# Kernel tuning notes

Measured on AMD Instinct MI355X. Metric: run time of the kernel, lower is better.

Reference implementation:

```python
import jax, jax.numpy as jnp
import numpy as np

B, PS, E, A, EMB, D, V, LC, TCAP = 128, 14, 2048, 512, 512, 512, 10000, 128, 26
T = TCAP - 1  # max decode length


def setup_inputs() -> dict:
    key = jax.random.key(0)
    ks = jax.random.split(key, 16)
    g = lambda k, shape: jax.random.normal(k, shape, jnp.float32) * 0.02
    cap_len = jax.random.randint(ks[2], (B, 1), 2, TCAP + 1).at[0, 0].set(TCAP)
    return {
        "encoder_out": jax.random.normal(ks[0], (B, PS, PS, E), jnp.float32),
        "encoded_captions": jax.random.randint(ks[1], (B, TCAP), 0, V),
        "caption_lengths": cap_len,
        "length_class": jax.random.randint(ks[3], (B,), 0, 3),
        "W_enc_att": g(ks[4], (E, A)), "b_enc_att": jnp.zeros((A,), jnp.float32),
        "W_dec_att": g(ks[5], (D, A)), "b_dec_att": jnp.zeros((A,), jnp.float32),
        "w_full_att": g(ks[6], (A,)), "b_full_att": jnp.zeros((), jnp.float32),
        "W_init_h": g(ks[7], (E, D)), "b_init_h": jnp.zeros((D,), jnp.float32),
        "W_init_c": g(ks[8], (E, D)), "b_init_c": jnp.zeros((D,), jnp.float32),
        "W_fbeta": g(ks[9], (D, E)), "b_fbeta": jnp.zeros((E,), jnp.float32),
        "emb_table": jax.random.uniform(ks[10], (V, EMB), jnp.float32, -0.1, 0.1),
        "lc_table": jax.random.uniform(ks[11], (3, LC), jnp.float32, -0.1, 0.1),
        "W_fc": jax.random.uniform(ks[12], (D, V), jnp.float32, -0.1, 0.1),
        "b_fc": jnp.zeros((V,), jnp.float32),
        "W_ih": g(ks[13], (EMB + E + LC, 4 * D)), "b_ih": jnp.zeros((4 * D,), jnp.float32),
        "W_hh": g(ks[14], (D, 4 * D)), "b_hh": jnp.zeros((4 * D,), jnp.float32),
    }


def reference(encoder_out, encoded_captions, caption_lengths, length_class,
              W_enc_att, b_enc_att, W_dec_att, b_dec_att, w_full_att, b_full_att,
              W_init_h, b_init_h, W_init_c, b_init_c, W_fbeta, b_fbeta,
              emb_table, lc_table, W_fc, b_fc, W_ih, b_ih, W_hh, b_hh):
    enc = encoder_out.reshape(B, -1, E)                      # [B, P, E]
    cap_len = caption_lengths[:, 0]
    sort_ind = jnp.argsort(-cap_len)                          # descending by length
    enc = enc[sort_ind]
    caps = encoded_captions[sort_ind]
    style = lc_table[length_class[sort_ind]]                  # [B, LC]
    dec_len = cap_len[sort_ind] - 1                           # [B]

    embs = emb_table[caps]                                    # [B, TCAP, EMB]
    mean_enc = enc.mean(axis=1)
    h0 = mean_enc @ W_init_h + b_init_h
    c0 = mean_enc @ W_init_c + b_init_c
    # encoder side of attention is time-invariant: precompute once
    att1 = jnp.einsum('bpe,ea->bpa', enc, W_enc_att) + b_enc_att

    def step(carry, xs):
        h, c = carry
        t, emb_t = xs
        att2 = h @ W_dec_att + b_dec_att
        e = jnp.einsum('bpa,a->bp', jax.nn.relu(att1 + att2[:, None, :]), w_full_att) + b_full_att
        alpha = jax.nn.softmax(e, axis=1)                     # [B, P]
        awe = jnp.einsum('bpe,bp->be', enc, alpha)
        gate = jax.nn.sigmoid(h @ W_fbeta + b_fbeta)
        x = jnp.concatenate([emb_t, style, gate * awe], axis=1)
        gates = x @ W_ih + b_ih + h @ W_hh + b_hh             # [B, 4D], order i,f,g,o
        i, f, g, o = jnp.split(gates, 4, axis=1)
        c_new = jax.nn.sigmoid(f) * c + jax.nn.sigmoid(i) * jnp.tanh(g)
        h_new = jax.nn.sigmoid(o) * jnp.tanh(c_new)
        preds = h_new @ W_fc + b_fc                           # dropout is identity in eval
        m = (t < dec_len)[:, None]                            # active sequences at step t
        return ((jnp.where(m, h_new, h), jnp.where(m, c_new, c)),
                (jnp.where(m, preds, 0.0), jnp.where(m, alpha, 0.0)))

    ts = jnp.arange(T)
    emb_seq = jnp.swapaxes(embs[:, :T, :], 0, 1)              # [T, B, EMB]
    _, (preds, alphas) = jax.lax.scan(step, (h0, c0), (ts, emb_seq))
    predictions = jnp.swapaxes(preds, 0, 1)                   # [B, T, V]
    alphas = jnp.swapaxes(alphas, 0, 1)                       # [B, T, P]
    return predictions, caps, dec_len, alphas, sort_ind
```

## Files before the change

### kernel.cpp

```cpp
#include <hip/hip_runtime.h>
#include <math.h>

constexpr int kB   = 128;
constexpr int kP   = 196;
constexpr int kPT  = 200;
constexpr int kE   = 2048;
constexpr int kA   = 512;
constexpr int kEMB = 512;
constexpr int kD   = 512;
constexpr int kV   = 10000;
constexpr int kLC  = 128;
constexpr int kTCAP= 26;
constexpr int kT   = 25;
constexpr int kX   = kEMB + kLC + kE;
constexpr int kXH  = kX + kD;
constexpr int kN3  = kV + kA + kE;
constexpr int kBIG = 1 << 30;
constexpr int KZ   = 5;

typedef __attribute__((ext_vector_type(8))) short bf8;
typedef __attribute__((ext_vector_type(4))) float f4;

__device__ inline float b2f(ushort u) { return __uint_as_float(((unsigned)u) << 16); }
__device__ inline ushort f2b(float f) {
    unsigned u = __float_as_uint(f);
    return (ushort)((u + 0x7fffu + ((u >> 16) & 1u)) >> 16);
}

#define SWZ(r, k) ((((r) * 32) + (k)) ^ (((r) & 7) << 3))

__global__ __launch_bounds__(128) void sort_setup(
    const int* __restrict__ caplen, const int* __restrict__ caps_in,
    const int* __restrict__ lclass, const float* __restrict__ lc_table,
    int* __restrict__ sort_ind, int* __restrict__ declen, int* __restrict__ caps_i,
    float* __restrict__ style,
    float* __restrict__ out_caps, float* __restrict__ out_declen,
    float* __restrict__ out_sortind)
{
    __shared__ int lens[kB];
    __shared__ int sind[kB];
    int i = threadIdx.x;
    lens[i] = caplen[i];
    __syncthreads();
    int li = lens[i];
    int r = 0;
    for (int j = 0; j < kB; j++) {
        int lj = lens[j];
        if (lj > li || (lj == li && j < i)) r++;
    }
    sind[r] = i;
    sort_ind[r] = i;
    out_sortind[r] = (float)i;
    __syncthreads();
    int orig = sind[i];
    int dl = lens[orig] - 1;
    declen[i] = dl;
    out_declen[i] = (float)dl;
    for (int t = 0; t < kTCAP; t++) {
        int cv = caps_in[orig * kTCAP + t];
        caps_i[i * kTCAP + t] = cv;
        out_caps[i * kTCAP + t] = (float)cv;
    }
    int lcl = lclass[orig];
    for (int k = 0; k < kLC; k++) style[i * kLC + k] = lc_table[lcl * kLC + k];
}

__global__ __launch_bounds__(256) void tcvt_kernel(
    const float* __restrict__ src, int ldsrc, int K, int N,
    ushort* __restrict__ dst, long long ldd)
{
    __shared__ float tile[32][33];
    int k0 = blockIdx.y * 32, n0 = blockIdx.x * 32;
    int tx = threadIdx.x & 31, ty = threadIdx.x >> 5;
    #pragma unroll
    for (int j = 0; j < 4; j++) {
        int k = k0 + ty + j * 8, n = n0 + tx;
        tile[ty + j * 8][tx] = (k < K && n < N) ? src[(long long)k * ldsrc + n] : 0.f;
    }
    __syncthreads();
    #pragma unroll
    for (int j = 0; j < 4; j++) {
        int n = n0 + ty + j * 8, k = k0 + tx;
        if (n < N && k < K) dst[(long long)n * ldd + k] = f2b(tile[tx][ty + j * 8]);
    }
}

__global__ __launch_bounds__(256) void bias_setup_kernel(
    const float* __restrict__ b_fc, const float* __restrict__ b_dec,
    const float* __restrict__ b_fb, const float* __restrict__ b_ih0,
    const float* __restrict__ b_ic0, const float* __restrict__ b_ih,
    const float* __restrict__ b_hh,
    float* __restrict__ bias3, float* __restrict__ bias_hc, float* __restrict__ gbias)
{
    int idx = blockIdx.x * 256 + threadIdx.x;
    if (idx < kN3) {
        float v;
        if (idx < kV) v = b_fc[idx];
        else if (idx < kV + kA) v = b_dec[idx - kV];
        else v = b_fb[idx - kV - kA];
        bias3[idx] = v;
    } else if (idx < kN3 + 1024) {
        int i = idx - kN3;
        bias_hc[i] = (i < 512) ? b_ih0[i] : b_ic0[i - 512];
    } else if (idx < kN3 + 1024 + 2048) {
        int i = idx - kN3 - 1024;
        gbias[i] = b_ih[i] + b_hh[i];
    }
}

__global__ __launch_bounds__(256) void enc_cvt_kernel(
    const float* __restrict__ enc, const int* __restrict__ sort_ind,
    ushort* __restrict__ enc_bf)
{
    long long idx4 = (long long)blockIdx.x * 256 + threadIdx.x;
    if (idx4 >= (long long)kB * kP * kE / 4) return;
    int r = (int)(idx4 >> 9);
    int cc = ((int)idx4 & 511) * 4;
    int b = r / kP, p = r - b * kP;
    long long srow = (long long)sort_ind[b] * kP + p;
    float4 v = *(const float4*)(enc + srow * kE + cc);
    ushort4 o; o.x = f2b(v.x); o.y = f2b(v.y); o.z = f2b(v.z); o.w = f2b(v.w);
    *(ushort4*)(enc_bf + (long long)r * kE + cc) = o;
}

__global__ __launch_bounds__(256) void encT_kernel(
    const ushort* __restrict__ enc_bf, ushort* __restrict__ enc_T)
{
    __shared__ ushort tile[kPT][65];
    int b = blockIdx.y, e0 = blockIdx.x * 64;
    int tid = threadIdx.x;
    tile[196 + (tid >> 6)][tid & 63] = 0;
    const ushort* src = enc_bf + (long long)b * kP * kE + e0;
    for (int idx = tid; idx < kP * 64; idx += 256) {
        int p = idx >> 6, j = idx & 63;
        tile[p][j] = src[(long long)p * kE + j];
    }
    __syncthreads();
    ushort* dst = enc_T + ((long long)b * kE + e0) * kPT;
    for (int j = 0; j < 64; j++) {
        if (tid < kPT) dst[(long long)j * kPT + tid] = tile[tid][j];
    }
}

__global__ __launch_bounds__(256) void mean_enc_kernel(
    const float* __restrict__ encf, const ushort* __restrict__ encb,
    const ushort* __restrict__ encT, int mode,
    const int* __restrict__ sort_ind, float* __restrict__ me)
{
    int idx = blockIdx.x * 256 + threadIdx.x;
    int b = idx >> 11, e = idx & 2047;
    float s = 0.f;
    if (mode == 2) {
        const ushort* base = encT + (long long)idx * kPT;
        #pragma unroll
        for (int i = 0; i < kPT / 8; i++) {
            uint4 u = *(const uint4*)(base + i * 8);
            const ushort* pu = (const ushort*)&u;
            #pragma unroll
            for (int j = 0; j < 8; j++) s += b2f(pu[j]);
        }
    } else if (mode == 1) {
        const ushort* base = encb + (long long)b * kP * kE + e;
        #pragma unroll 4
        for (int p = 0; p < kP; p++) s += b2f(base[(long long)p * kE]);
    } else {
        const float* base = encf + (long long)sort_ind[b] * kP * kE + e;
        #pragma unroll 4
        for (int p = 0; p < kP; p++) s += base[(long long)p * kE];
    }
    me[idx] = s * (1.0f / 196.0f);
}

__global__ __launch_bounds__(256) void gemm2(
    const void* __restrict__ Am, int lda, int a_bf16,
    const ushort* __restrict__ Bt, int ldbt,
    const float* __restrict__ bias,
    void* __restrict__ out1, long long ldc1, int c1_bf16,
    int split1, float* __restrict__ out2, long long ldc2,
    int split2, float* __restrict__ out3, long long ldc3,
    const int* __restrict__ declen, int t, int pred_mode,
    int M, int N, int K, long long zstride)
{
    __shared__ short As[64 * 32];
    __shared__ short Bs[128 * 32];
    int tid = threadIdx.x;
    int lane = tid & 63, w = tid >> 6, quad = lane >> 4, l16 = lane & 15;
    int m0 = blockIdx.y * 64, n0 = blockIdx.x * 128;

    f4 acc[8];
    #pragma unroll
    for (int i = 0; i < 8; i++) acc[i] = (f4){0.f, 0.f, 0.f, 0.f};

    int a_r = tid >> 2;
    int a_kc = (tid & 3) * 8;
    long long a_row = m0 + a_r;
    const float*  a_srcf = (const float*)Am  + a_row * (long long)lda + a_kc;
    const ushort* a_srcb = (const ushort*)Am + a_row * (long long)lda + a_kc;

    int b_r = tid >> 1;
    int b_kc = (tid & 1) * 16;
    bool bvalid = (n0 + b_r) < N;
    const ushort* b_src = Bt + (long long)(n0 + b_r) * ldbt + b_kc;

    int kpb = K / (int)gridDim.z;
    int kbeg = (int)blockIdx.z * kpb, kend = kbeg + kpb;

    float4 af0 = make_float4(0.f, 0.f, 0.f, 0.f), af1 = af0;
    uint4 au, bu0, bu1;
    au.x = au.y = au.z = au.w = 0u; bu0 = au; bu1 = au;

    if (a_bf16) au = *(const uint4*)(a_srcb + kbeg);
    else { af0 = *(const float4*)(a_srcf + kbeg); af1 = *(const float4*)(a_srcf + kbeg + 4); }
    if (bvalid) { bu0 = *(const uint4*)(b_src + kbeg); bu1 = *(const uint4*)(b_src + kbeg + 8); }

    for (int k0 = kbeg; k0 < kend; k0 += 32) {
        __syncthreads();
        if (a_bf16) {
            *(uint4*)&As[SWZ(a_r, a_kc)] = au;
        } else {
            uint4 pk; ushort* pp = (ushort*)&pk;
            pp[0] = f2b(af0.x); pp[1] = f2b(af0.y); pp[2] = f2b(af0.z); pp[3] = f2b(af0.w);
            pp[4] = f2b(af1.x); pp[5] = f2b(af1.y); pp[6] = f2b(af1.z); pp[7] = f2b(af1.w);
            *(uint4*)&As[SWZ(a_r, a_kc)] = pk;
        }
        *(uint4*)&Bs[SWZ(b_r, b_kc)]     = bu0;
        *(uint4*)&Bs[SWZ(b_r, b_kc + 8)] = bu1;
        int kn = k0 + 32;
        if (kn < kend) {
            if (a_bf16) au = *(const uint4*)(a_srcb + kn);
            else { af0 = *(const float4*)(a_srcf + kn); af1 = *(const float4*)(a_srcf + kn + 4); }
            if (bvalid) { bu0 = *(const uint4*)(b_src + kn); bu1 = *(const uint4*)(b_src + kn + 8); }
        }
        __syncthreads();
        bf8 a = *(const bf8*)&As[SWZ(w * 16 + l16, quad * 8)];
        #pragma unroll
        for (int nt = 0; nt < 8; nt++) {
            bf8 b = *(const bf8*)&Bs[SWZ(nt * 16 + l16, quad * 8)];
            acc[nt] = __builtin_amdgcn_mfma_f32_16x16x32_bf16(a, b, acc[nt], 0, 0, 0);
        }
    }

    long long zoff = (long long)blockIdx.z * zstride;
    #pragma unroll
    for (int nt = 0; nt < 8; nt++) {
        int cn = n0 + nt * 16 + l16;
        if (cn >= N) continue;
        float bv = bias ? bias[cn] : 0.f;
        #pragma unroll
        for (int reg = 0; reg < 4; reg++) {
            int rr = m0 + w * 16 + quad * 4 + reg;
            float v = acc[nt][reg] + bv;
            if (cn < split1) {
                long long idx;
                if (pred_mode) {
                    int bb = rr & 127, tt = rr >> 7;
                    if (tt >= declen[bb]) v = 0.f;
                    idx = ((long long)bb * kT + tt) * ldc1 + cn;
                } else {
                    if (declen && t >= declen[rr]) v = 0.f;
                    idx = (long long)rr * ldc1 + cn + zoff;
                }
                if (c1_bf16) ((ushort*)out1)[idx] = f2b(v);
                else         ((float*)out1)[idx] = v;
            } else if (cn < split2) {
                out2[(long long)rr * ldc2 + (cn - split1)] = v;
            } else {
                out3[(long long)rr * ldc3 + (cn - split2)] = v;
            }
        }
    }
}

__global__ __launch_bounds__(256) void gemm_big(
    const ushort* __restrict__ A, int lda,
    const ushort* __restrict__ Bt, int ldbt,
    const float* __restrict__ bias,
    void* __restrict__ out1, long long ldc1, int c1_bf16,
    const int* __restrict__ declen, int pred_mode,
    int M, int N, int K)
{
    __shared__ short As[128 * 32];
    __shared__ short Bs[128 * 32];
    unsigned nwg = gridDim.x * gridDim.y;
    unsigned lin = blockIdx.y * gridDim.x + blockIdx.x;
    unsigned q = nwg >> 3, rm = nwg & 7;
    unsigned xcd = lin & 7, loc = lin >> 3;
    unsigned swz = (xcd < rm ? xcd * (q + 1) : rm * (q + 1) + (xcd - rm) * q) + loc;
    int bx = (int)(swz % gridDim.x), by = (int)(swz / gridDim.x);
    int m0 = by * 128, n0 = bx * 128;

    int tid = threadIdx.x;
    int lane = tid & 63, w = tid >> 6, quad = lane >> 4, l16 = lane & 15;
    int wr = w >> 1, wc = w & 1;

    f4 acc[4][4];
    #pragma unroll
    for (int m = 0; m < 4; m++)
        #pragma unroll
        for (int n = 0; n < 4; n++) acc[m][n] = (f4){0.f, 0.f, 0.f, 0.f};

    bool wact = true;
    if (pred_mode) wact = declen[wr * 64] > (m0 >> 7);

    int s_r = tid >> 1, s_kc = (tid & 1) * 16;
    const ushort* a_src = A + (long long)(m0 + s_r) * lda + s_kc;
    bool bval = (n0 + s_r) < N;
    const ushort* b_src = Bt + (long long)(n0 + s_r) * ldbt + s_kc;

    uint4 au0, au1, bu0, bu1;
    au0.x = au0.y = au0.z = au0.w = 0u; au1 = au0; bu0 = au0; bu1 = au0;
    au0 = *(const uint4*)(a_src);
    au1 = *(const uint4*)(a_src + 8);
    if (bval) { bu0 = *(const uint4*)(b_src); bu1 = *(const uint4*)(b_src + 8); }

    for (int k0 = 0; k0 < K; k0 += 32) {
        __syncthreads();
        *(uint4*)&As[SWZ(s_r, s_kc)]     = au0;
        *(uint4*)&As[SWZ(s_r, s_kc + 8)] = au1;
        *(uint4*)&Bs[SWZ(s_r, s_kc)]     = bu0;
        *(uint4*)&Bs[SWZ(s_r, s_kc + 8)] = bu1;
        int kn = k0 + 32;
        if (kn < K) {
            au0 = *(const uint4*)(a_src + kn);
            au1 = *(const uint4*)(a_src + kn + 8);
            if (bval) { bu0 = *(const uint4*)(b_src + kn); bu1 = *(const uint4*)(b_src + kn + 8); }
        }
        __syncthreads();
        if (wact) {
            bf8 af[4], bfr[4];
            #pragma unroll
            for (int m = 0; m < 4; m++)
                af[m] = *(const bf8*)&As[SWZ(wr * 64 + m * 16 + l16, quad * 8)];
            #pragma unroll
            for (int n = 0; n < 4; n++)
                bfr[n] = *(const bf8*)&Bs[SWZ(wc * 64 + n * 16 + l16, quad * 8)];
            #pragma unroll
            for (int m = 0; m < 4; m++)
                #pragma unroll
                for (int n = 0; n < 4; n++)
                    acc[m][n] = __builtin_amdgcn_mfma_f32_16x16x32_bf16(af[m], bfr[n], acc[m][n], 0, 0, 0);
        }
    }

    #pragma unroll
    for (int n = 0; n < 4; n++) {
        int cn = n0 + wc * 64 + n * 16 + l16;
        if (cn >= N) continue;
        float bv = bias ? bias[cn] : 0.f;
        #pragma unroll
        for (int m = 0; m < 4; m++) {
            #pragma unroll
            for (int reg = 0; reg < 4; reg++) {
                int rr = m0 + wr * 64 + m * 16 + quad * 4 + reg;
                float v = acc[m][n][reg] + bv;
                long long idx;
                if (pred_mode) {
                    int bb = rr & 127, tt = rr >> 7;
                    if (tt >= declen[bb]) v = 0.f;
                    idx = ((long long)bb * kT + tt) * ldc1 + cn;
                } else {
                    idx = (long long)rr * ldc1 + cn;
                }
                if (c1_bf16) ((ushort*)out1)[idx] = f2b(v);
                else         ((float*)out1)[idx] = v;
            }
        }
    }
}

__global__ __launch_bounds__(512) void attn_awe_kernel(
    const ushort* __restrict__ att1, const float* __restrict__ att2,
    const float* __restrict__ w_full, const float* __restrict__ b_full,
    const float* __restrict__ encf, const ushort* __restrict__ encb,
    const ushort* __restrict__ encT, int mode,
    const int* __restrict__ sort_ind, const float* __restrict__ gate,
    const int* __restrict__ caps_i, int t,
    const float* __restrict__ emb_table, const float* __restrict__ style,
    ushort* __restrict__ xh, float* __restrict__ alphas_out,
    const int* __restrict__ declen, const int* __restrict__ smap)
{
    int b = blockIdx.y;
    int half = blockIdx.x;
    int ob = smap ? smap[b] : b;
    __shared__ float al[kPT];
    __shared__ float red1[8], red2[8];
    int tid = threadIdx.x, wave = tid >> 6, lane = tid & 63;

    float a2r[8], wfr[8];
    {
        const float4* ap = (const float4*)(att2 + (long long)b * kA + lane * 8);
        *(float4*)&a2r[0] = ap[0]; *(float4*)&a2r[4] = ap[1];
        const float4* wp = (const float4*)(w_full + lane * 8);
        *(float4*)&wfr[0] = wp[0]; *(float4*)&wfr[4] = wp[1];
    }
    float bfull = b_full[0];
    const ushort* a1 = att1 + (long long)ob * kP * kA + lane * 8;
    for (int i0 = 0; i0 < 25; i0 += 4) {
        uint4 u[4]; int pv[4];
        #pragma unroll
        for (int j = 0; j < 4; j++) {
            int i = i0 + j, p = wave + 8 * i;
            pv[j] = (i < 25 && p < kP) ? p : -1;
            if (pv[j] >= 0) u[j] = *(const uint4*)(a1 + (long long)pv[j] * kA);
        }
        #pragma unroll
        for (int j = 0; j < 4; j++) {
            if (pv[j] < 0) continue;
            const unsigned* uw = (const unsigned*)&u[j];
            float s = 0.f;
            #pragma unroll
            for (int q = 0; q < 4; q++) {
                unsigned x = uw[q];
                float v0 = b2f((ushort)(x & 0xffffu)) + a2r[2 * q];
                float v1 = b2f((ushort)(x >> 16))     + a2r[2 * q + 1];
                s += fmaxf(v0, 0.f) * wfr[2 * q] + fmaxf(v1, 0.f) * wfr[2 * q + 1];
            }
            #pragma unroll
            for (int off = 32; off; off >>= 1) s += __shfl_down(s, off);
            if (lane == 0) al[pv[j]] = s + bfull;
        }
    }
    __syncthreads();

    float e = (tid < kP) ? al[tid] : -1e30f;
    float wm = e;
    for (int off = 32; off; off >>= 1) wm = fmaxf(wm, __shfl_down(wm, off));
    if (lane == 0) red1[wave] = wm;
    __syncthreads();
    float gm = red1[0];
    #pragma unroll
    for (int i = 1; i < 8; i++) gm = fmaxf(gm, red1[i]);
    float ex = (tid < kP) ? expf(e - gm) : 0.f;
    float sw = ex;
    for (int off = 32; off; off >>= 1) sw += __shfl_down(sw, off);
    if (lane == 0) red2[wave] = sw;
    __syncthreads();
    float S = red2[0];
    #pragma unroll
    for (int i = 1; i < 8; i++) S += red2[i];
    float a = ex / S;
    __syncthreads();
    if (tid < kP) {
        al[tid] = a;
        if (half == 0)
            alphas_out[((long long)b * kT + t) * kP + tid] = (t < declen[b]) ? a : 0.f;
    } else if (tid < kPT) {
        al[tid] = 0.f;
    }
    __syncthreads();

    if (half == 1 && tid < 160) {
        int tok = caps_i[b * kTCAP + t];
        float4 v;
        if (tid < 128) v = *(const float4*)(emb_table + (long long)tok * kEMB + tid * 4);
        else           v = *(const float4*)(style + b * kLC + (tid - 128) * 4);
        ushort4 o; o.x = f2b(v.x); o.y = f2b(v.y); o.z = f2b(v.z); o.w = f2b(v.w);
        *(ushort4*)(xh + (long long)b * kXH + tid * 4) = o;
    }

    int c0 = half * 1024 + tid * 2;
    float s0 = 0.f, s1 = 0.f;
    if (mode == 2) {
        const ushort* r0 = encT + ((long long)b * kE + c0) * kPT;
        const ushort* r1 = r0 + kPT;
        #pragma unroll 5
        for (int i = 0; i < kPT / 8; i++) {
            uint4 ua = *(const uint4*)(r0 + i * 8);
            uint4 ub = *(const uint4*)(r1 + i * 8);
            f4 alo = *(const f4*)&al[i * 8];
            f4 ahi = *(const f4*)&al[i * 8 + 4];
            const ushort* pa = (const ushort*)&ua;
            const ushort* pb = (const ushort*)&ub;
            s0 += b2f(pa[0]) * alo.x + b2f(pa[1]) * alo.y + b2f(pa[2]) * alo.z + b2f(pa[3]) * alo.w;
            s0 += b2f(pa[4]) * ahi.x + b2f(pa[5]) * ahi.y + b2f(pa[6]) * ahi.z + b2f(pa[7]) * ahi.w;
            s1 += b2f(pb[0]) * alo.x + b2f(pb[1]) * alo.y + b2f(pb[2]) * alo.z + b2f(pb[3]) * alo.w;
            s1 += b2f(pb[4]) * ahi.x + b2f(pb[5]) * ahi.y + b2f(pb[6]) * ahi.z + b2f(pb[7]) * ahi.w;
        }
    } else if (mode == 1) {
        const ushort* base = encb + (long long)b * kP * kE + c0;
        #pragma unroll 4
        for (int p = 0; p < kP; p++) {
            unsigned uu = *(const unsigned*)(base + (long long)p * kE);
            float ap = al[p];
            s0 += b2f((ushort)(uu & 0xffffu)) * ap;
            s1 += b2f((ushort)(uu >> 16))     * ap;
        }
    } else {
        const float* base = encf + (long long)sort_ind[b] * kP * kE + c0;
        #pragma unroll 4
        for (int p = 0; p < kP; p++) {
            float2 v = *(const float2*)(base + (long long)p * kE);
            float ap = al[p];
            s0 += v.x * ap; s1 += v.y * ap;
        }
    }
    float2 g = *(const float2*)(gate + (long long)b * kE + c0);
    float o0 = s0 / (1.f + expf(-g.x));
    float o1 = s1 / (1.f + expf(-g.y));
    unsigned pw = (unsigned)f2b(o0) | ((unsigned)f2b(o1) << 16);
    *(unsigned*)(xh + (long long)b * kXH + kEMB + kLC + c0) = pw;
}

__global__ __launch_bounds__(256) void lstm_cell_kernel(
    const float* __restrict__ gpart, const float* __restrict__ gbias,
    ushort* __restrict__ xh, float* __restrict__ c,
    ushort* __restrict__ Hbuf, int t)
{
    int idx = blockIdx.x * 256 + threadIdx.x;
    int b = idx >> 9, d = idx & 511;
    float gi = gbias[d], gf = gbias[kD + d], gg = gbias[2 * kD + d], go = gbias[3 * kD + d];
    const float* g = gpart + (long long)b * 4 * kD + d;
    #pragma unroll
    for (int z = 0; z < KZ; z++) {
        const float* gz = g + (long long)z * kB * 4 * kD;
        gi += gz[0]; gf += gz[kD]; gg += gz[2 * kD]; go += gz[3 * kD];
    }
    float si = 1.f / (1.f + expf(-gi));
    float sf = 1.f / (1.f + expf(-gf));
    float so = 1.f / (1.f + expf(-go));
    float cn = sf * c[idx] + si * tanhf(gg);
    float hn = so * tanhf(cn);
    c[idx] = cn;
    ushort hb = f2b(hn);
    xh[(long long)b * kXH + kX + d] = hb;
    Hbuf[((long long)t * kB + b) * kD + d] = hb;
}

extern "C" void kernel_launch(void* const* d_in, const int* in_sizes, int n_in,
                              void* d_out, int out_size, void* d_ws, size_t ws_size,
                              hipStream_t stream)
{
    const float* encoder_out  = (const float*)d_in[0];
    const int*   enc_caps     = (const int*)  d_in[1];
    const int*   cap_lengths  = (const int*)  d_in[2];
    const int*   length_class = (const int*)  d_in[3];
    const float* W_enc_att = (const float*)d_in[4];
    const float* b_enc_att = (const float*)d_in[5];
    const float* W_dec_att = (const float*)d_in[6];
    const float* b_dec_att = (const float*)d_in[7];
    const float* w_full_att = (const float*)d_in[8];
    const float* b_full_att = (const float*)d_in[9];
    const float* W_init_h = (const float*)d_in[10];
    const float* b_init_h = (const float*)d_in[11];
    const float* W_init_c = (const float*)d_in[12];
    const float* b_init_c = (const float*)d_in[13];
    const float* W_fbeta  = (const float*)d_in[14];
    const float* b_fbeta  = (const float*)d_in[15];
    const float* emb_table = (const float*)d_in[16];
    const float* lc_table  = (const float*)d_in[17];
    const float* W_fc = (const float*)d_in[18];
    const float* b_fc = (const float*)d_in[19];
    const float* W_ih = (const float*)d_in[20];
    const float* b_ih = (const float*)d_in[21];
    const float* W_hh = (const float*)d_in[22];
    const float* b_hh = (const float*)d_in[23];

    float* out = (float*)d_out;
    float* o_pred    = out;
    float* o_caps    = out + (long long)kB * kT * kV;
    float* o_declen  = o_caps + kB * kTCAP;
    float* o_alpha   = o_declen + kB;
    float* o_sortind = o_alpha + (long long)kB * kT * kP;

    float* w = (float*)d_ws;
    float* c        = w; w += kB * kD;
    float* att2     = w; w += kB * kA;
    float* gate     = w; w += kB * kE;
    float* mean_enc = w; w += kB * kE;
    float* gpart    = w; w += (long long)kB * 4 * kD * KZ;
    float* style    = w; w += kB * kLC;
    float* bias3    = w; w += kN3;
    float* bias_hc  = w; w += 1024;
    float* gbias    = w; w += 2048;
    ushort* us = (ushort*)w;
    ushort* xh_bf    = us; us += (long long)kB * kXH;
    ushort* att1_bf  = us; us += (long long)kB * kP * kA;
    ushort* WencT    = us; us += (long long)kA * kE;
    ushort* WhcT     = us; us += (long long)1024 * kE;
    ushort* WcatT    = us; us += (long long)(4 * kD) * kXH;
    ushort* Wcat3T   = us; us += (long long)kN3 * kD;
    ushort* Hbuf     = us; us += (long long)kT * kB * kD;
    int* iw = (int*)us;
    int* sort_ind = iw; iw += kB;
    int* declen   = iw; iw += kB;
    int* caps_i   = iw; iw += kB * kTCAP;
    ushort* enc_bf = (ushort*)(iw + kB);
    ushort* enc_T  = enc_bf + (long long)kB * kP * kE;

    size_t need_encbf = ((char*)(enc_bf + (long long)kB * kP * kE)) - (char*)d_ws;
    size_t need_encT  = ((char*)(enc_T  + (long long)kB * kE * kPT)) - (char*)d_ws;
    int use_encbf = (ws_size >= need_encbf) ? 1 : 0;
    int use_encT  = (ws_size >= need_encT) ? 1 : 0;
    int mode = use_encT ? 2 : (use_encbf ? 1 : 0);

    sort_setup<<<1, 128, 0, stream>>>(cap_lengths, enc_caps, length_class, lc_table,
        sort_ind, declen, caps_i, style, o_caps, o_declen, o_sortind);

    auto tc = [&](const float* s, int ldsrc, int Kr, int Nc, ushort* d, long long ldd) {
        tcvt_kernel<<<dim3((Nc + 31) / 32, (Kr + 31) / 32), 256, 0, stream>>>(
            s, ldsrc, Kr, Nc, d, ldd);
    };
    tc(W_enc_att, kA, kE, kA, WencT, kE);
    tc(W_init_h,  kD, kE, kD, WhcT, kE);
    tc(W_init_c,  kD, kE, kD, WhcT + (long long)kD * kE, kE);
    tc(W_ih, 4 * kD, kX, 4 * kD, WcatT, kXH);
    tc(W_hh, 4 * kD, kD, 4 * kD, WcatT + kX, kXH);
    tc(W_fc,      kV, kD, kV, Wcat3T, kD);
    tc(W_dec_att, kA, kD, kA, Wcat3T + (long long)kV * kD, kD);
    tc(W_fbeta,   kE, kD, kE, Wcat3T + (long long)(kV + kA) * kD, kD);
    bias_setup_kernel<<<(kN3 + 1024 + 2048 + 255) / 256, 256, 0, stream>>>(
        b_fc, b_dec_att, b_fbeta, b_init_h, b_init_c, b_ih, b_hh, bias3, bias_hc, gbias);

    if (use_encbf) {
        enc_cvt_kernel<<<(unsigned)(((long long)kB * kP * kE / 4 + 255) / 256), 256, 0, stream>>>(
            encoder_out, sort_ind, enc_bf);
    }
    if (use_encT) {
        encT_kernel<<<dim3(kE / 64, kB), 256, 0, stream>>>(enc_bf, enc_T);
    }
    mean_enc_kernel<<<(kB * kE) / 256, 256, 0, stream>>>(
        encoder_out, enc_bf, enc_T, mode, sort_ind, mean_enc);

    auto g2 = [](int M, int N) { return dim3((unsigned)((N + 127) / 128), (unsigned)(M / 64)); };

    gemm2<<<g2(kB, 1024), 256, 0, stream>>>(mean_enc, kE, 0, WhcT, kE, bias_hc,
        xh_bf + kX, kXH, 1, 512, c, kD, kBIG, nullptr, 0, nullptr, 0, 0,
        kB, 1024, kE, 0);

    if (use_encbf) {
        gemm_big<<<dim3(kA / 128, kB * kP / 128), 256, 0, stream>>>(
            enc_bf, kE, WencT, kE, b_enc_att,
            att1_bf, kA, 1, nullptr, 0, kB * kP, kA, kE);
    } else {
        gemm2<<<g2(kB * kP, kA), 256, 0, stream>>>(encoder_out, kE, 0, WencT, kE, b_enc_att,
            att1_bf, kA, 1, kBIG, nullptr, 0, kBIG, nullptr, 0, nullptr, 0, 0,
            kB * kP, kA, kE, 0);
    }

    gemm2<<<g2(kB, kA + kE), 256, 0, stream>>>(xh_bf + kX, kXH, 1,
        Wcat3T + (long long)kV * kD, kD, bias3 + kV, att2, kA, 0,
        kA, gate, kE, kBIG, nullptr, 0, nullptr, 0, 0, kB, kA + kE, kD, 0);

    const int* smap = use_encbf ? nullptr : sort_ind;
    for (int t = 0; t < kT; t++) {
        attn_awe_kernel<<<dim3(2, kB), 512, 0, stream>>>(att1_bf, att2, w_full_att,
            b_full_att, encoder_out, enc_bf, enc_T, mode, sort_ind, gate, caps_i, t,
            emb_table, style, xh_bf, o_alpha, declen, smap);
        gemm2<<<dim3((4 * kD + 127) / 128, kB / 64, KZ), 256, 0, stream>>>(
            xh_bf, kXH, 1, WcatT, kXH, nullptr,
            gpart, 4 * kD, 0, kBIG, nullptr, 0, kBIG, nullptr, 0, nullptr, 0, 0,
            kB, 4 * kD, kXH, (long long)kB * 4 * kD);
        lstm_cell_kernel<<<(kB * kD) / 256, 256, 0, stream>>>(gpart, gbias, xh_bf, c, Hbuf, t);
        gemm2<<<g2(kB, kA + kE), 256, 0, stream>>>(xh_bf + kX, kXH, 1,
            Wcat3T + (long long)kV * kD, kD, bias3 + kV, att2, kA, 0,
            kA, gate, kE, kBIG, nullptr, 0, nullptr, 0, 0, kB, kA + kE, kD, 0);
    }

    gemm_big<<<dim3((kV + 127) / 128, kT * kB / 128), 256, 0, stream>>>(
        Hbuf, kD, Wcat3T, kD, bias3,
        o_pred, kV, 0, declen, 1, kT * kB, kV, kD);
}
```

Before: 2.634 ms.

## Split attention into energy and AWE kernels; stage fp32 GEMM epilogue through LDS

The fused attention kernel, which ran 2 blocks per batch row, is split into an energy kernel and a softmax+AWE kernel. The old design had each of the 2 blocks recompute all 196 energies. Now energy work is divided across halves and AWE runs on 9 blocks per row, which exposes more parallelism. The fp32 output path of gemm_big (the large prediction GEMM) now stages tiles through shared memory so it can do coalesced float4 stores instead of scattered scalar stores. The cost is an extra kernel launch per step and a global round-trip for the energies, plus added LDS and syncs in the GEMM epilogue.

```diff
diff --git a/kernel.cpp b/kernel.cpp
--- a/kernel.cpp
+++ b/kernel.cpp
@@ -281,6 +281,7 @@
 {
     __shared__ short As[128 * 32];
     __shared__ short Bs[128 * 32];
+    __shared__ float Cs[128][33];
     unsigned nwg = gridDim.x * gridDim.y;
     unsigned lin = blockIdx.y * gridDim.x + blockIdx.x;
     unsigned q = nwg >> 3, rm = nwg & 7;
@@ -342,163 +343,190 @@
         }
     }
 
-    #pragma unroll
-    for (int n = 0; n < 4; n++) {
-        int cn = n0 + wc * 64 + n * 16 + l16;
-        if (cn >= N) continue;
-        float bv = bias ? bias[cn] : 0.f;
-        #pragma unroll
-        for (int m = 0; m < 4; m++) {
-            #pragma unroll
-            for (int reg = 0; reg < 4; reg++) {
-                int rr = m0 + wr * 64 + m * 16 + quad * 4 + reg;
-                float v = acc[m][n][reg] + bv;
+    if (c1_bf16) {
+        #pragma unroll
+        for (int n = 0; n < 4; n++) {
+            int cn = n0 + wc * 64 + n * 16 + l16;
+            if (cn >= N) continue;
+            float bv = bias ? bias[cn] : 0.f;
+            #pragma unroll
+            for (int m = 0; m < 4; m++) {
+                #pragma unroll
+                for (int reg = 0; reg < 4; reg++) {
+                    int rr = m0 + wr * 64 + m * 16 + quad * 4 + reg;
+                    float v = acc[m][n][reg] + bv;
+                    long long idx;
+                    if (pred_mode) {
+                        int bb = rr & 127, tt = rr >> 7;
+                        if (tt >= declen[bb]) v = 0.f;
+                        idx = ((long long)bb * kT + tt) * ldc1 + cn;
+                    } else {
+                        idx = (long long)rr * ldc1 + cn;
+                    }
+                    ((ushort*)out1)[idx] = f2b(v);
+                }
+            }
+        }
+    } else {
+        #pragma unroll
+        for (int ch = 0; ch < 4; ch++) {
+            __syncthreads();
+            if (wc == (ch >> 1)) {
+                #pragma unroll
+                for (int nn = 0; nn < 2; nn++) {
+                    int n = (ch & 1) * 2 + nn;
+                    int cn = n0 + wc * 64 + n * 16 + l16;
+                    float bv = bias ? bias[cn] : 0.f;
+                    #pragma unroll
+                    for (int m = 0; m < 4; m++) {
+                        int r = wr * 64 + m * 16 + quad * 4;
+                        #pragma unroll
+                        for (int reg = 0; reg < 4; reg++)
+                            Cs[r + reg][nn * 16 + l16] = acc[m][n][reg] + bv;
+                    }
+                }
+            }
+            __syncthreads();
+            int ccol0 = n0 + (ch >> 1) * 64 + (ch & 1) * 32;
+            int tr = tid >> 3;
+            int tc = (tid & 7) * 4;
+            #pragma unroll
+            for (int rr4 = 0; rr4 < 4; rr4++) {
+                int r = rr4 * 32 + tr;
+                int grow = m0 + r;
+                int cn = ccol0 + tc;
+                if (cn >= N) continue;
+                float4 v = *(const float4*)&Cs[r][tc];
                 long long idx;
                 if (pred_mode) {
-                    int bb = rr & 127, tt = rr >> 7;
-                    if (tt >= declen[bb]) v = 0.f;
+                    int bb = grow & 127, tt = grow >> 7;
+                    if (tt >= declen[bb]) v = make_float4(0.f, 0.f, 0.f, 0.f);
                     idx = ((long long)bb * kT + tt) * ldc1 + cn;
                 } else {
-                    idx = (long long)rr * ldc1 + cn;
+                    idx = (long long)grow * ldc1 + cn;
                 }
-                if (c1_bf16) ((ushort*)out1)[idx] = f2b(v);
-                else         ((float*)out1)[idx] = v;
+                *(float4*)((float*)out1 + idx) = v;
             }
         }
     }
 }
 
-__global__ __launch_bounds__(512) void attn_awe_kernel(
+__global__ __launch_bounds__(512) void energy_kernel(
     const ushort* __restrict__ att1, const float* __restrict__ att2,
     const float* __restrict__ w_full, const float* __restrict__ b_full,
+    float* __restrict__ es, const int* __restrict__ smap)
+{
+    int b = blockIdx.y, half = blockIdx.x;
+    int ob = smap ? smap[b] : b;
+    int tid = threadIdx.x, wave = tid >> 6, lane = tid & 63;
+    float a2r[8], wfr[8];
+    {
+        const float4* ap = (const float4*)(att2 + (long long)b * kA + lane * 8);
+        *(float4*)&a2r[0] = ap[0]; *(float4*)&a2r[4] = ap[1];
+        const float4* wp = (const float4*)(w_full + lane * 8);
+        *(float4*)&wfr[0] = wp[0]; *(float4*)&wfr[4] = wp[1];
+    }
+    float bfull = b_full[0];
+    int p0 = half * 98;
+    const ushort* a1 = att1 + ((long long)ob * kP + p0) * kA + lane * 8;
+    for (int i0 = 0; i0 < 13; i0 += 4) {
+        uint4 u[4]; int pl[4];
+        #pragma unroll
+        for (int j = 0; j < 4; j++) {
+            int i = i0 + j, p = wave + 8 * i;
+            pl[j] = (i < 13 && p < 98) ? p : -1;
+            if (pl[j] >= 0) u[j] = *(const uint4*)(a1 + (long long)pl[j] * kA);
+        }
+        #pragma unroll
+        for (int j = 0; j < 4; j++) {
+            if (pl[j] < 0) continue;
+            const unsigned* uw = (const unsigned*)&u[j];
+            float s = 0.f;
+            #pragma unroll
+            for (int qq = 0; qq < 4; qq++) {
+                unsigned x = uw[qq];
+                float v0 = b2f((ushort)(x & 0xffffu)) + a2r[2 * qq];
+                float v1 = b2f((ushort)(x >> 16))     + a2r[2 * qq + 1];
+                s += fmaxf(v0, 0.f) * wfr[2 * qq] + fmaxf(v1, 0.f) * wfr[2 * qq + 1];
+            }
+            #pragma unroll
+            for (int off = 32; off; off >>= 1) s += __shfl_down(s, off);
+            if (lane == 0) es[b * kP + p0 + pl[j]] = s + bfull;
+        }
+    }
+}
+
+__global__ __launch_bounds__(256) void awe_kernel(
+    const float* __restrict__ es,
     const float* __restrict__ encf, const ushort* __restrict__ encb,
     const ushort* __restrict__ encT, int mode,
     const int* __restrict__ sort_ind, const float* __restrict__ gate,
     const int* __restrict__ caps_i, int t,
     const float* __restrict__ emb_table, const float* __restrict__ style,
     ushort* __restrict__ xh, float* __restrict__ alphas_out,
-    const int* __restrict__ declen, const int* __restrict__ smap)
-{
-    int b = blockIdx.y;
-    int half = blockIdx.x;
-    int ob = smap ? smap[b] : b;
+    const int* __restrict__ declen)
+{
+    int b = blockIdx.y, x = blockIdx.x;
     __shared__ float al[kPT];
-    __shared__ float red1[8], red2[8];
+    __shared__ float red1[4], red2[4];
     int tid = threadIdx.x, wave = tid >> 6, lane = tid & 63;
 
-    float a2r[8], wfr[8];
-    {
-        const float4* ap = (const float4*)(att2 + (long long)b * kA + lane * 8);
-        *(float4*)&a2r[0] = ap[0]; *(float4*)&a2r[4] = ap[1];
-        const float4* wp = (const float4*)(w_full + lane * 8);
-        *(float4*)&wfr[0] = wp[0]; *(float4*)&wfr[4] = wp[1];
-    }
-    float bfull = b_full[0];
-    const ushort* a1 = att1 + (long long)ob * kP * kA + lane * 8;
-    for (int i0 = 0; i0 < 25; i0 += 4) {
-        uint4 u[4]; int pv[4];
-        #pragma unroll
-        for (int j = 0; j < 4; j++) {
-            int i = i0 + j, p = wave + 8 * i;
-            pv[j] = (i < 25 && p < kP) ? p : -1;
-            if (pv[j] >= 0) u[j] = *(const uint4*)(a1 + (long long)pv[j] * kA);
-        }
-        #pragma unroll
-        for (int j = 0; j < 4; j++) {
-            if (pv[j] < 0) continue;
-            const unsigned* uw = (const unsigned*)&u[j];
-            float s = 0.f;
-            #pragma unroll
-            for (int q = 0; q < 4; q++) {
-                unsigned x = uw[q];
-                float v0 = b2f((ushort)(x & 0xffffu)) + a2r[2 * q];
-                float v1 = b2f((ushort)(x >> 16))     + a2r[2 * q + 1];
-                s += fmaxf(v0, 0.f) * wfr[2 * q] + fmaxf(v1, 0.f) * wfr[2 * q + 1];
-            }
-            #pragma unroll
-            for (int off = 32; off; off >>= 1) s += __shfl_down(s, off);
-            if (lane == 0) al[pv[j]] = s + bfull;
-        }
-    }
-    __syncthreads();
-
-    float e = (tid < kP) ? al[tid] : -1e30f;
+    float e = (tid < kP) ? es[b * kP + tid] : -1e30f;
     float wm = e;
     for (int off = 32; off; off >>= 1) wm = fmaxf(wm, __shfl_down(wm, off));
     if (lane == 0) red1[wave] = wm;
     __syncthreads();
-    float gm = red1[0];
-    #pragma unroll
-    for (int i = 1; i < 8; i++) gm = fmaxf(gm, red1[i]);
+    float gm = fmaxf(fmaxf(red1[0], red1[1]), fmaxf(red1[2], red1[3]));
     float ex = (tid < kP) ? expf(e - gm) : 0.f;
     float sw = ex;
     for (int off = 32; off; off >>= 1) sw += __shfl_down(sw, off);
     if (lane == 0) red2[wave] = sw;
     __syncthreads();
-    float S = red2[0];
-    #pragma unroll
-    for (int i = 1; i < 8; i++) S += red2[i];
+    float S = red2[0] + red2[1] + red2[2] + red2[3];
     float a = ex / S;
+    if (tid < kP) al[tid] = a;
+    else if (tid < kPT) al[tid] = 0.f;
     __syncthreads();
-    if (tid < kP) {
-        al[tid] = a;
-        if (half == 0)
+
+    if (x == 8) {
+        if (tid < kP)
             alphas_out[((long long)b * kT + t) * kP + tid] = (t < declen[b]) ? a : 0.f;
-    } else if (tid < kPT) {
-        al[tid] = 0.f;
-    }
-    __syncthreads();
-
-    if (half == 1 && tid < 160) {
         int tok = caps_i[b * kTCAP + t];
-        float4 v;
-        if (tid < 128) v = *(const float4*)(emb_table + (long long)tok * kEMB + tid * 4);
-        else           v = *(const float4*)(style + b * kLC + (tid - 128) * 4);
-        ushort4 o; o.x = f2b(v.x); o.y = f2b(v.y); o.z = f2b(v.z); o.w = f2b(v.w);
-        *(ushort4*)(xh + (long long)b * kXH + tid * 4) = o;
-    }
-
-    int c0 = half * 1024 + tid * 2;
-    float s0 = 0.f, s1 = 0.f;
+        for (int i = tid; i < 160; i += 256) {
+            float4 v;
+            if (i < 128) v = *(const float4*)(emb_table + (long long)tok * kEMB + i * 4);
+            else         v = *(const float4*)(style + b * kLC + (i - 128) * 4);
+            ushort4 o; o.x = f2b(v.x); o.y = f2b(v.y); o.z = f2b(v.z); o.w = f2b(v.w);
+            *(ushort4*)(xh + (long long)b * kXH + i * 4) = o;
+        }
+        return;
+    }
+
+    int c = x * 256 + tid;
+    float s = 0.f;
     if (mode == 2) {
-        const ushort* r0 = encT + ((long long)b * kE + c0) * kPT;
-        const ushort* r1 = r0 + kPT;
+        const ushort* r = encT + ((long long)b * kE + c) * kPT;
         #pragma unroll 5
         for (int i = 0; i < kPT / 8; i++) {
-            uint4 ua = *(const uint4*)(r0 + i * 8);
-            uint4 ub = *(const uint4*)(r1 + i * 8);
+            uint4 u = *(const uint4*)(r + i * 8);
+            const ushort* pu = (const ushort*)&u;
             f4 alo = *(const f4*)&al[i * 8];
             f4 ahi = *(const f4*)&al[i * 8 + 4];
-            const ushort* pa = (const ushort*)&ua;
-            const ushort* pb = (const ushort*)&ub;
-            s0 += b2f(pa[0]) * alo.x + b2f(pa[1]) * alo.y + b2f(pa[2]) * alo.z + b2f(pa[3]) * alo.w;
-            s0 += b2f(pa[4]) * ahi.x + b2f(pa[5]) * ahi.y + b2f(pa[6]) * ahi.z + b2f(pa[7]) * ahi.w;
-            s1 += b2f(pb[0]) * alo.x + b2f(pb[1]) * alo.y + b2f(pb[2]) * alo.z + b2f(pb[3]) * alo.w;
-            s1 += b2f(pb[4]) * ahi.x + b2f(pb[5]) * ahi.y + b2f(pb[6]) * ahi.z + b2f(pb[7]) * ahi.w;
+            s += b2f(pu[0]) * alo.x + b2f(pu[1]) * alo.y + b2f(pu[2]) * alo.z + b2f(pu[3]) * alo.w;
+            s += b2f(pu[4]) * ahi.x + b2f(pu[5]) * ahi.y + b2f(pu[6]) * ahi.z + b2f(pu[7]) * ahi.w;
         }
     } else if (mode == 1) {
-        const ushort* base = encb + (long long)b * kP * kE + c0;
+        const ushort* base = encb + (long long)b * kP * kE + c;
         #pragma unroll 4
-        for (int p = 0; p < kP; p++) {
-            unsigned uu = *(const unsigned*)(base + (long long)p * kE);
-            float ap = al[p];
-            s0 += b2f((ushort)(uu & 0xffffu)) * ap;
-            s1 += b2f((ushort)(uu >> 16))     * ap;
-        }
+        for (int p = 0; p < kP; p++) s += b2f(base[(long long)p * kE]) * al[p];
     } else {
-        const float* base = encf + (long long)sort_ind[b] * kP * kE + c0;
+        const float* base = encf + (long long)sort_ind[b] * kP * kE + c;
         #pragma unroll 4
-        for (int p = 0; p < kP; p++) {
-            float2 v = *(const float2*)(base + (long long)p * kE);
-            float ap = al[p];
-            s0 += v.x * ap; s1 += v.y * ap;
-        }
-    }
-    float2 g = *(const float2*)(gate + (long long)b * kE + c0);
-    float o0 = s0 / (1.f + expf(-g.x));
-    float o1 = s1 / (1.f + expf(-g.y));
-    unsigned pw = (unsigned)f2b(o0) | ((unsigned)f2b(o1) << 16);
-    *(unsigned*)(xh + (long long)b * kXH + kEMB + kLC + c0) = pw;
+        for (int p = 0; p < kP; p++) s += base[(long long)p * kE] * al[p];
+    }
+    float g = gate[(long long)b * kE + c];
+    float o = s / (1.f + expf(-g));
+    xh[(long long)b * kXH + kEMB + kLC + c] = f2b(o);
 }
 
 __global__ __launch_bounds__(256) void lstm_cell_kernel(
@@ -568,6 +596,7 @@
     float* gate     = w; w += kB * kE;
     float* mean_enc = w; w += kB * kE;
     float* gpart    = w; w += (long long)kB * 4 * kD * KZ;
+    float* es       = w; w += kB * kP;
     float* style    = w; w += kB * kLC;
     float* bias3    = w; w += kN3;
     float* bias_hc  = w; w += 1024;
@@ -643,9 +672,10 @@
 
     const int* smap = use_encbf ? nullptr : sort_ind;
     for (int t = 0; t < kT; t++) {
-        attn_awe_kernel<<<dim3(2, kB), 512, 0, stream>>>(att1_bf, att2, w_full_att,
-            b_full_att, encoder_out, enc_bf, enc_T, mode, sort_ind, gate, caps_i, t,
-            emb_table, style, xh_bf, o_alpha, declen, smap);
+        energy_kernel<<<dim3(2, kB), 512, 0, stream>>>(att1_bf, att2, w_full_att,
+            b_full_att, es, smap);
+        awe_kernel<<<dim3(9, kB), 256, 0, stream>>>(es, encoder_out, enc_bf, enc_T,
+            mode, sort_ind, gate, caps_i, t, emb_table, style, xh_bf, o_alpha, declen);
         gemm2<<<dim3((4 * kD + 127) / 128, kB / 64, KZ), 256, 0, stream>>>(
             xh_bf, kXH, 1, WcatT, kXH, nullptr,
             gpart, 4 * kD, 0, kBIG, nullptr, 0, kBIG, nullptr, 0, nullptr, 0, 0,
```

New measurement: 2.443 ms. -7.3%, faster.
